# Kernel tuning notes

Measured on AMD Instinct MI355X. Metric: run time of the kernel, lower is better.

Reference implementation:

```python
import jax, jax.numpy as jnp
import numpy as np

B, N, D, K, S = 256, 100000, 768, 5, 256
EPS = 1e-8  # F.cosine_similarity eps


def setup_inputs() -> dict:
    key = jax.random.key(0)
    ks = jax.random.split(key, 6)
    content_features = jax.random.normal(ks[0], (B, D), jnp.float32)
    target_speaker_id = jax.random.randint(ks[1], (B,), 0, S, dtype=jnp.int64)
    training_features = jax.random.normal(ks[2], (N, D), jnp.float32)
    speaker_ids = jax.random.randint(ks[3], (N,), 0, S, dtype=jnp.int64)
    W1 = jax.random.normal(ks[4], (2 * D, D), jnp.float32) * 0.02
    b1 = jnp.zeros((D,), jnp.float32)
    W2 = jax.random.normal(ks[5], (D, D), jnp.float32) * 0.02
    b2 = jnp.zeros((D,), jnp.float32)
    return {
        "content_features": content_features,
        "target_speaker_id": target_speaker_id,
        "training_features": training_features,
        "speaker_ids": speaker_ids,
        "W1": W1, "b1": b1, "W2": W2, "b2": b2,
    }


def reference(content_features, target_speaker_id, training_features, speaker_ids, W1, b1, W2, b2):
    # Cosine similarity of each query against the full memory bank (vectorized
    # version of the per-sample torch loop; speaker mask applied via -inf fill).
    qn = content_features / jnp.maximum(
        jnp.linalg.norm(content_features, axis=-1, keepdims=True), EPS)
    cn = training_features / jnp.maximum(
        jnp.linalg.norm(training_features, axis=-1, keepdims=True), EPS)
    sims = jnp.einsum('bd,nd->bn', qn, cn)                     # [B, N]
    same_spk = speaker_ids[None, :] == target_speaker_id[:, None]  # [B, N]
    masked = jnp.where(same_spk, sims, jnp.float32(-1e30))
    _, top_idx = jax.lax.top_k(masked, K)                      # [B, K]
    retrieved = training_features[top_idx].mean(axis=1)        # [B, D]
    combined = jnp.concatenate([content_features, retrieved], axis=-1)  # [B, 2D]
    # enhance_net (dropout p=0.05 is identity at inference)
    h = jax.nn.silu(combined @ W1 + b1)
    enhanced = h @ W2 + b2
    # Samples with no same-speaker candidate pass through unchanged.
    has_match = same_spk.any(axis=1, keepdims=True)
    return jnp.where(has_match, enhanced, content_features)
```

## Files before the change

kernel.cpp:

```cpp
#include <hip/hip_runtime.h>
#include <hip/hip_bf16.h>
#include <math.h>

#define DIM 768
#define KSEL 5
#define NSPK 256
#define BCAP 2048
#define GSPLIT 8
#define NSLICE (GSPLIT * 4)
#define SK1 16
#define SK2 12
#define SCAT_ITEMS 4

__global__ __launch_bounds__(1024)
void scatter_hist_kernel(const int* __restrict__ spk, int n,
                         int* __restrict__ cursor, int* __restrict__ bucket) {
    __shared__ int hist[NSPK];
    __shared__ int base[NSPK];
    const int tid = threadIdx.x;
    const int i0  = blockIdx.x * (1024 * SCAT_ITEMS);

    if (tid < NSPK) hist[tid] = 0;
    __syncthreads();

    int s_[SCAT_ITEMS], r_[SCAT_ITEMS];
#pragma unroll
    for (int j = 0; j < SCAT_ITEMS; ++j) {
        int i = i0 + tid + j * 1024;
        if (i < n) {
            int s = spk[i];
            s_[j] = s;
            r_[j] = atomicAdd(&hist[s], 1);
        } else {
            s_[j] = -1; r_[j] = 0;
        }
    }
    __syncthreads();

    if (tid < NSPK) base[tid] = hist[tid] ? atomicAdd(&cursor[tid], hist[tid]) : 0;
    __syncthreads();

#pragma unroll
    for (int j = 0; j < SCAT_ITEMS; ++j) {
        int i = i0 + tid + j * 1024;
        if (i < n) {
            int s = s_[j];
            int p = base[s] + r_[j];
            if (p < BCAP) bucket[(size_t)s * BCAP + p] = i;
        }
    }
}

__global__ __launch_bounds__(256)
void topk_partial_kernel(const float* __restrict__ content,
                         const int* __restrict__ target_spk,
                         const float* __restrict__ train,
                         const int* __restrict__ counts,
                         const int* __restrict__ bucket,
                         float* __restrict__ pvals,
                         int* __restrict__ pidx) {
    const int b    = blockIdx.x;
    const int g    = blockIdx.y;
    const int tid  = threadIdx.x;
    const int lane = tid & 63;
    const int wave = tid >> 6;
    const int slice = g * 4 + wave;

    const float4* q4 = (const float4*)(content + (size_t)b * DIM);
    const float4 q0 = q4[lane], q1 = q4[lane + 64], q2 = q4[lane + 128];

    const int spk = target_spk[b];
    const int cnt = min(counts[spk], BCAP);
    const int* buck = bucket + (size_t)spk * BCAP;

    float tv[KSEL] = {-3.0e38f, -3.0e38f, -3.0e38f, -3.0e38f, -3.0e38f};
    int   ti[KSEL] = {-1, -1, -1, -1, -1};

    int c = slice;
    int rowA = (c < cnt) ? buck[c] : -1;
    int rowB = (c + NSLICE < cnt) ? buck[c + NSLICE] : -1;

    for (; c < cnt; c += 2 * NSLICE) {
        const int curA = rowA;
        const int curB = rowB;
        const bool has2 = (curB >= 0);
        const float4* ra = (const float4*)(train + (size_t)curA * DIM);
        const float4* rb = (const float4*)(train + (size_t)(has2 ? curB : curA) * DIM);

        float4 a0 = ra[lane], a1 = ra[lane + 64], a2 = ra[lane + 128];
        float4 b0 = rb[lane], b1 = rb[lane + 64], b2 = rb[lane + 128];

        const int cn = c + 2 * NSLICE;
        rowA = (cn < cnt) ? buck[cn] : -1;
        rowB = (cn + NSLICE < cnt) ? buck[cn + NSLICE] : -1;

        float dA = 0.f, cA = 0.f, dB = 0.f, cB = 0.f;
        dA += a0.x*q0.x + a0.y*q0.y + a0.z*q0.z + a0.w*q0.w;
        cA += a0.x*a0.x + a0.y*a0.y + a0.z*a0.z + a0.w*a0.w;
        dB += b0.x*q0.x + b0.y*q0.y + b0.z*q0.z + b0.w*q0.w;
        cB += b0.x*b0.x + b0.y*b0.y + b0.z*b0.z + b0.w*b0.w;
        dA += a1.x*q1.x + a1.y*q1.y + a1.z*q1.z + a1.w*q1.w;
        cA += a1.x*a1.x + a1.y*a1.y + a1.z*a1.z + a1.w*a1.w;
        dB += b1.x*q1.x + b1.y*q1.y + b1.z*q1.z + b1.w*q1.w;
        cB += b1.x*b1.x + b1.y*b1.y + b1.z*b1.z + b1.w*b1.w;
        dA += a2.x*q2.x + a2.y*q2.y + a2.z*q2.z + a2.w*q2.w;
        cA += a2.x*a2.x + a2.y*a2.y + a2.z*a2.z + a2.w*a2.w;
        dB += b2.x*q2.x + b2.y*q2.y + b2.z*q2.z + b2.w*q2.w;
        cB += b2.x*b2.x + b2.y*b2.y + b2.z*b2.z + b2.w*b2.w;

#pragma unroll
        for (int off = 32; off; off >>= 1) {
            dA += __shfl_xor(dA, off);
            cA += __shfl_xor(cA, off);
            dB += __shfl_xor(dB, off);
            cB += __shfl_xor(cB, off);
        }
        const float keyA = dA * rsqrtf(cA);
        const float keyB = dB * rsqrtf(cB);

        if (keyA > tv[KSEL - 1]) {
#pragma unroll
            for (int j = 0; j < KSEL; ++j)
                if (keyA > tv[j]) {
                    for (int m = KSEL - 1; m > j; --m) { tv[m] = tv[m-1]; ti[m] = ti[m-1]; }
                    tv[j] = keyA; ti[j] = curA;
                    break;
                }
        }
        if (has2 && keyB > tv[KSEL - 1]) {
#pragma unroll
            for (int j = 0; j < KSEL; ++j)
                if (keyB > tv[j]) {
                    for (int m = KSEL - 1; m > j; --m) { tv[m] = tv[m-1]; ti[m] = ti[m-1]; }
                    tv[j] = keyB; ti[j] = curB;
                    break;
                }
        }
    }

    if (lane == 0) {
        float* pv = pvals + ((size_t)b * NSLICE + slice) * KSEL;
        int*   pi = pidx  + ((size_t)b * NSLICE + slice) * KSEL;
#pragma unroll
        for (int j = 0; j < KSEL; ++j) { pv[j] = tv[j]; pi[j] = ti[j]; }
    }
}

__global__ __launch_bounds__(256)
void merge_retrieve_kernel(const float* __restrict__ content,
                           const int* __restrict__ target_spk,
                           const float* __restrict__ train,
                           const int* __restrict__ spk_ids,
                           const int* __restrict__ counts,
                           const float* __restrict__ pvals,
                           const int* __restrict__ pidx,
                           float* __restrict__ combined,
                           int* __restrict__ flags,
                           int nTrain) {
    __shared__ float mv[NSLICE * KSEL];
    __shared__ int   mi[NSLICE * KSEL];
    __shared__ int   sel[KSEL];
    const int b = blockIdx.x, tid = threadIdx.x;
    const int NP = NSLICE * KSEL;

    for (int i = tid; i < NP; i += 256) {
        mv[i] = pvals[(size_t)b * NP + i];
        mi[i] = pidx[(size_t)b * NP + i];
    }
    __syncthreads();

    if (tid < 64) {
        const int l = tid;
        float L0 = mv[l];
        float L1 = mv[l + 64];
        float L2 = (l < 32) ? mv[l + 128] : -3.4e38f;
#pragma unroll
        for (int j = 0; j < KSEL; ++j) {
            float bv = L0; int code = l;
            if (L1 > bv) { bv = L1; code = l + 64; }
            if (L2 > bv) { bv = L2; code = l + 128; }
#pragma unroll
            for (int off = 32; off; off >>= 1) {
                float ov = __shfl_xor(bv, off);
                int   oc = __shfl_xor(code, off);
                if (ov > bv) { bv = ov; code = oc; }
            }
            if ((code & 63) == l) {
                if (code < 64) L0 = -3.4e38f;
                else if (code < 128) L1 = -3.4e38f;
                else L2 = -3.4e38f;
            }
            if (l == 0) sel[j] = (bv > -1.0e37f) ? mi[code] : -1;
        }
    }
    __syncthreads();

    if (tid == 0) {
        const int spk = target_spk[b];
        const int cnt = counts[spk];
        flags[b] = (cnt > 0) ? 1 : 0;
        if (cnt < KSEL) {
            int fill = 0;
            for (int j = 0; j < KSEL; ++j) if (sel[j] < 0) {
                while (fill < nTrain && spk_ids[fill] == spk) ++fill;
                sel[j] = (fill < nTrain) ? fill : 0;
                ++fill;
            }
        }
    }
    __syncthreads();

    const int s0 = sel[0], s1 = sel[1], s2 = sel[2], s3 = sel[3], s4 = sel[4];
    const float* qrow = content + (size_t)b * DIM;
    float* crow = combined + (size_t)b * 2 * DIM;
    for (int d = tid; d < DIM; d += 256) {
        float acc = train[(size_t)s0 * DIM + d] + train[(size_t)s1 * DIM + d]
                  + train[(size_t)s2 * DIM + d] + train[(size_t)s3 * DIM + d]
                  + train[(size_t)s4 * DIM + d];
        crow[d]       = qrow[d];
        crow[DIM + d] = acc * 0.2f;
    }
}

__global__ __launch_bounds__(256)
void gemm_partial_kernel(const float* __restrict__ A, const float* __restrict__ W,
                         float* __restrict__ part, int M, int Nc, int Kd, int KS) {
    __shared__ float As[32][68];
    __shared__ float Ws[32][68];
    const int tid  = threadIdx.x;
    const int col0 = blockIdx.x * 64;
    const int row0 = blockIdx.y * 64;
    const int sk   = blockIdx.z;
    const int kbase = sk * KS;
    const int ty4 = (tid >> 4) << 2;
    const int tx4 = (tid & 15) << 2;

    float acc[4][4] = {};

    for (int kt = 0; kt < KS; kt += 32) {
        const int k0 = kbase + kt;
#pragma unroll
        for (int i = 0; i < 2; ++i) {
            int idx = tid + 256 * i;
            int r   = idx >> 3;
            int kq  = (idx & 7) << 2;
            float4 v = *(const float4*)&A[(size_t)(row0 + r) * Kd + k0 + kq];
            As[kq + 0][r] = v.x; As[kq + 1][r] = v.y;
            As[kq + 2][r] = v.z; As[kq + 3][r] = v.w;
        }
#pragma unroll
        for (int i = 0; i < 2; ++i) {
            int idx = tid + 256 * i;
            int kr  = idx >> 4;
            int c4  = (idx & 15) << 2;
            *(float4*)&Ws[kr][c4] = *(const float4*)&W[(size_t)(k0 + kr) * Nc + col0 + c4];
        }
        __syncthreads();
#pragma unroll
        for (int k = 0; k < 32; ++k) {
            float4 av = *(const float4*)&As[k][ty4];
            float4 wv = *(const float4*)&Ws[k][tx4];
            float a_[4] = {av.x, av.y, av.z, av.w};
            float w_[4] = {wv.x, wv.y, wv.z, wv.w};
#pragma unroll
            for (int i = 0; i < 4; ++i)
#pragma unroll
                for (int j = 0; j < 4; ++j) acc[i][j] += a_[i] * w_[j];
        }
        __syncthreads();
    }

    float* p = part + ((size_t)sk * M + row0) * Nc + col0;
#pragma unroll
    for (int i = 0; i < 4; ++i) {
        float4 o = make_float4(acc[i][0], acc[i][1], acc[i][2], acc[i][3]);
        *(float4*)&p[(size_t)(ty4 + i) * Nc + tx4] = o;
    }
}

template <int ACT, bool SELECT, int NSK>
__global__ __launch_bounds__(256)
void combine_kernel(const float* __restrict__ part, const float* __restrict__ bias,
                    float* __restrict__ out, int M, int Nc,
                    const int* __restrict__ flags, const float* __restrict__ pass) {
    const int i = blockIdx.x * 256 + threadIdx.x;
    if (i >= M * Nc) return;
    const int row = i / Nc;
    const int col = i - row * Nc;
    float v = bias[col];
#pragma unroll
    for (int s = 0; s < NSK; ++s) v += part[(size_t)s * M * Nc + i];
    if (ACT == 1) v = v / (1.0f + expf(-v));
    if (SELECT && !flags[row]) v = pass[i];
    out[i] = v;
}

extern "C" void kernel_launch(void* const* d_in, const int* in_sizes, int n_in,
                              void* d_out, int out_size, void* d_ws, size_t ws_size,
                              hipStream_t stream) {
    const float* content = (const float*)d_in[0];
    const int*   target  = (const int*)d_in[1];
    const float* train   = (const float*)d_in[2];
    const int*   spk     = (const int*)d_in[3];
    const float* W1      = (const float*)d_in[4];
    const float* b1      = (const float*)d_in[5];
    const float* W2      = (const float*)d_in[6];
    const float* b2      = (const float*)d_in[7];
    float* out = (float*)d_out;

    const int B = in_sizes[1];
    const int N = in_sizes[3];

    char* w = (char*)d_ws;
    size_t off = 0;
    auto alloc = [&](size_t bytes) -> void* {
        off = (off + 255) & ~(size_t)255;
        void* p = w + off;
        off += bytes;
        return p;
    };
    int*   cursor   = (int*)alloc(NSPK * sizeof(int));
    int*   bucket   = (int*)alloc((size_t)NSPK * BCAP * sizeof(int));
    int*   flags    = (int*)alloc((size_t)B * sizeof(int));
    float* pvals    = (float*)alloc((size_t)B * NSLICE * KSEL * sizeof(float));
    int*   pidx     = (int*)alloc((size_t)B * NSLICE * KSEL * sizeof(int));
    float* combined = (float*)alloc((size_t)B * 2 * DIM * sizeof(float));
    float* hbuf     = (float*)alloc((size_t)B * DIM * sizeof(float));
    float* part1    = (float*)alloc((size_t)SK1 * B * DIM * sizeof(float));
    float* part2    = (float*)alloc((size_t)SK2 * B * DIM * sizeof(float));
    (void)ws_size;

    hipMemsetAsync(cursor, 0, NSPK * sizeof(int), stream);
    const int scat_blocks = (N + 1024 * SCAT_ITEMS - 1) / (1024 * SCAT_ITEMS);
    scatter_hist_kernel<<<scat_blocks, 1024, 0, stream>>>(spk, N, cursor, bucket);

    topk_partial_kernel<<<dim3(B, GSPLIT), 256, 0, stream>>>(
        content, target, train, cursor, bucket, pvals, pidx);
    merge_retrieve_kernel<<<B, 256, 0, stream>>>(
        content, target, train, spk, cursor, pvals, pidx, combined, flags, N);

    gemm_partial_kernel<<<dim3(DIM / 64, B / 64, SK1), 256, 0, stream>>>(
        combined, W1, part1, B, DIM, 2 * DIM, 2 * DIM / SK1);
    combine_kernel<1, false, SK1><<<(B * DIM + 255) / 256, 256, 0, stream>>>(
        part1, b1, hbuf, B, DIM, nullptr, nullptr);
    gemm_partial_kernel<<<dim3(DIM / 64, B / 64, SK2), 256, 0, stream>>>(
        hbuf, W2, part2, B, DIM, DIM, DIM / SK2);
    combine_kernel<0, true, SK2><<<(B * DIM + 255) / 256, 256, 0, stream>>>(
        part2, b2, out, B, DIM, flags, content);
}
```

Before: 136.1 us.

## Group queries by speaker so each candidate-row scan serves two queries

The scatter kernel now also builds a per-speaker list of query indices. The top-k kernel is relaunched over speakers instead of queries, and each wave scores two queries of the same speaker against every candidate row it loads. The goal is to cut repeated reads of the same speaker's training rows when several queries share a speaker, and to reuse each row norm across both queries. The cost is uneven work: speakers with no queries exit at once, while speakers with three or more queries loop over their rows again, which can lengthen the critical path.

```diff
diff --git a/kernel.cpp b/kernel.cpp
--- a/kernel.cpp
+++ b/kernel.cpp
@@ -6,6 +6,7 @@
 #define KSEL 5
 #define NSPK 256
 #define BCAP 2048
+#define QCAP 256
 #define GSPLIT 8
 #define NSLICE (GSPLIT * 4)
 #define SK1 16
@@ -14,11 +15,19 @@
 
 __global__ __launch_bounds__(1024)
 void scatter_hist_kernel(const int* __restrict__ spk, int n,
-                         int* __restrict__ cursor, int* __restrict__ bucket) {
+                         int* __restrict__ cursor, int* __restrict__ bucket,
+                         const int* __restrict__ target, int B,
+                         int* __restrict__ qcnt, int* __restrict__ qlist) {
     __shared__ int hist[NSPK];
     __shared__ int base[NSPK];
     const int tid = threadIdx.x;
     const int i0  = blockIdx.x * (1024 * SCAT_ITEMS);
+
+    if (blockIdx.x == 0 && tid < B) {
+        int s = target[tid];
+        int p = atomicAdd(&qcnt[s], 1);
+        qlist[(size_t)s * QCAP + p] = tid;
+    }
 
     if (tid < NSPK) hist[tid] = 0;
     __syncthreads();
@@ -52,97 +61,148 @@
 }
 
 __global__ __launch_bounds__(256)
-void topk_partial_kernel(const float* __restrict__ content,
-                         const int* __restrict__ target_spk,
-                         const float* __restrict__ train,
-                         const int* __restrict__ counts,
-                         const int* __restrict__ bucket,
-                         float* __restrict__ pvals,
-                         int* __restrict__ pidx) {
-    const int b    = blockIdx.x;
-    const int g    = blockIdx.y;
+void topk_spk_kernel(const float* __restrict__ content,
+                     const float* __restrict__ train,
+                     const int* __restrict__ counts,
+                     const int* __restrict__ bucket,
+                     const int* __restrict__ qcnt,
+                     const int* __restrict__ qlist,
+                     float* __restrict__ pvals,
+                     int* __restrict__ pidx) {
+    const int s  = blockIdx.x;
+    const int qn = qcnt[s];
+    if (qn == 0) return;
+
     const int tid  = threadIdx.x;
     const int lane = tid & 63;
     const int wave = tid >> 6;
-    const int slice = g * 4 + wave;
-
-    const float4* q4 = (const float4*)(content + (size_t)b * DIM);
-    const float4 q0 = q4[lane], q1 = q4[lane + 64], q2 = q4[lane + 128];
-
-    const int spk = target_spk[b];
-    const int cnt = min(counts[spk], BCAP);
-    const int* buck = bucket + (size_t)spk * BCAP;
-
-    float tv[KSEL] = {-3.0e38f, -3.0e38f, -3.0e38f, -3.0e38f, -3.0e38f};
-    int   ti[KSEL] = {-1, -1, -1, -1, -1};
-
-    int c = slice;
-    int rowA = (c < cnt) ? buck[c] : -1;
-    int rowB = (c + NSLICE < cnt) ? buck[c + NSLICE] : -1;
-
-    for (; c < cnt; c += 2 * NSLICE) {
-        const int curA = rowA;
-        const int curB = rowB;
-        const bool has2 = (curB >= 0);
-        const float4* ra = (const float4*)(train + (size_t)curA * DIM);
-        const float4* rb = (const float4*)(train + (size_t)(has2 ? curB : curA) * DIM);
-
-        float4 a0 = ra[lane], a1 = ra[lane + 64], a2 = ra[lane + 128];
-        float4 b0 = rb[lane], b1 = rb[lane + 64], b2 = rb[lane + 128];
-
-        const int cn = c + 2 * NSLICE;
-        rowA = (cn < cnt) ? buck[cn] : -1;
-        rowB = (cn + NSLICE < cnt) ? buck[cn + NSLICE] : -1;
-
-        float dA = 0.f, cA = 0.f, dB = 0.f, cB = 0.f;
-        dA += a0.x*q0.x + a0.y*q0.y + a0.z*q0.z + a0.w*q0.w;
-        cA += a0.x*a0.x + a0.y*a0.y + a0.z*a0.z + a0.w*a0.w;
-        dB += b0.x*q0.x + b0.y*q0.y + b0.z*q0.z + b0.w*q0.w;
-        cB += b0.x*b0.x + b0.y*b0.y + b0.z*b0.z + b0.w*b0.w;
-        dA += a1.x*q1.x + a1.y*q1.y + a1.z*q1.z + a1.w*q1.w;
-        cA += a1.x*a1.x + a1.y*a1.y + a1.z*a1.z + a1.w*a1.w;
-        dB += b1.x*q1.x + b1.y*q1.y + b1.z*q1.z + b1.w*q1.w;
-        cB += b1.x*b1.x + b1.y*b1.y + b1.z*b1.z + b1.w*b1.w;
-        dA += a2.x*q2.x + a2.y*q2.y + a2.z*q2.z + a2.w*q2.w;
-        cA += a2.x*a2.x + a2.y*a2.y + a2.z*a2.z + a2.w*a2.w;
-        dB += b2.x*q2.x + b2.y*q2.y + b2.z*q2.z + b2.w*q2.w;
-        cB += b2.x*b2.x + b2.y*b2.y + b2.z*b2.z + b2.w*b2.w;
-
-#pragma unroll
-        for (int off = 32; off; off >>= 1) {
-            dA += __shfl_xor(dA, off);
-            cA += __shfl_xor(cA, off);
-            dB += __shfl_xor(dB, off);
-            cB += __shfl_xor(cB, off);
-        }
-        const float keyA = dA * rsqrtf(cA);
-        const float keyB = dB * rsqrtf(cB);
-
-        if (keyA > tv[KSEL - 1]) {
-#pragma unroll
-            for (int j = 0; j < KSEL; ++j)
-                if (keyA > tv[j]) {
-                    for (int m = KSEL - 1; m > j; --m) { tv[m] = tv[m-1]; ti[m] = ti[m-1]; }
-                    tv[j] = keyA; ti[j] = curA;
-                    break;
+    const int slice = blockIdx.y * 4 + wave;
+
+    const int cnt = min(counts[s], BCAP);
+    const int* buck = bucket + (size_t)s * BCAP;
+
+    for (int c0 = 0; c0 < qn; c0 += 2) {
+        const int bq0   = qlist[(size_t)s * QCAP + c0];
+        const bool hasq1 = (c0 + 1 < qn);
+        const int bq1   = hasq1 ? qlist[(size_t)s * QCAP + c0 + 1] : bq0;
+
+        const float4* q0p = (const float4*)(content + (size_t)bq0 * DIM);
+        const float4* q1p = (const float4*)(content + (size_t)bq1 * DIM);
+        const float4 p0 = q0p[lane], p1 = q0p[lane + 64], p2 = q0p[lane + 128];
+        const float4 r0 = q1p[lane], r1 = q1p[lane + 64], r2 = q1p[lane + 128];
+
+        float tv0[KSEL] = {-3.0e38f, -3.0e38f, -3.0e38f, -3.0e38f, -3.0e38f};
+        int   ti0[KSEL] = {-1, -1, -1, -1, -1};
+        float tv1[KSEL] = {-3.0e38f, -3.0e38f, -3.0e38f, -3.0e38f, -3.0e38f};
+        int   ti1[KSEL] = {-1, -1, -1, -1, -1};
+
+        int c = slice;
+        int rowA = (c < cnt) ? buck[c] : -1;
+        int rowB = (c + NSLICE < cnt) ? buck[c + NSLICE] : -1;
+
+        for (; c < cnt; c += 2 * NSLICE) {
+            const int curA = rowA;
+            const int curB = rowB;
+            const bool has2 = (curB >= 0);
+            const float4* ra = (const float4*)(train + (size_t)curA * DIM);
+            const float4* rb = (const float4*)(train + (size_t)(has2 ? curB : curA) * DIM);
+
+            float4 xa0 = ra[lane], xa1 = ra[lane + 64], xa2 = ra[lane + 128];
+            float4 xb0 = rb[lane], xb1 = rb[lane + 64], xb2 = rb[lane + 128];
+
+            const int cn = c + 2 * NSLICE;
+            rowA = (cn < cnt) ? buck[cn] : -1;
+            rowB = (cn + NSLICE < cnt) ? buck[cn + NSLICE] : -1;
+
+            float dA0 = 0.f, dA1 = 0.f, cA = 0.f;
+            float dB0 = 0.f, dB1 = 0.f, cB = 0.f;
+
+            dA0 += xa0.x*p0.x + xa0.y*p0.y + xa0.z*p0.z + xa0.w*p0.w;
+            dA1 += xa0.x*r0.x + xa0.y*r0.y + xa0.z*r0.z + xa0.w*r0.w;
+            cA  += xa0.x*xa0.x + xa0.y*xa0.y + xa0.z*xa0.z + xa0.w*xa0.w;
+            dB0 += xb0.x*p0.x + xb0.y*p0.y + xb0.z*p0.z + xb0.w*p0.w;
+            dB1 += xb0.x*r0.x + xb0.y*r0.y + xb0.z*r0.z + xb0.w*r0.w;
+            cB  += xb0.x*xb0.x + xb0.y*xb0.y + xb0.z*xb0.z + xb0.w*xb0.w;
+
+            dA0 += xa1.x*p1.x + xa1.y*p1.y + xa1.z*p1.z + xa1.w*p1.w;
+            dA1 += xa1.x*r1.x + xa1.y*r1.y + xa1.z*r1.z + xa1.w*r1.w;
+            cA  += xa1.x*xa1.x + xa1.y*xa1.y + xa1.z*xa1.z + xa1.w*xa1.w;
+            dB0 += xb1.x*p1.x + xb1.y*p1.y + xb1.z*p1.z + xb1.w*p1.w;
+            dB1 += xb1.x*r1.x + xb1.y*r1.y + xb1.z*r1.z + xb1.w*r1.w;
+            cB  += xb1.x*xb1.x + xb1.y*xb1.y + xb1.z*xb1.z + xb1.w*xb1.w;
+
+            dA0 += xa2.x*p2.x + xa2.y*p2.y + xa2.z*p2.z + xa2.w*p2.w;
+            dA1 += xa2.x*r2.x + xa2.y*r2.y + xa2.z*r2.z + xa2.w*r2.w;
+            cA  += xa2.x*xa2.x + xa2.y*xa2.y + xa2.z*xa2.z + xa2.w*xa2.w;
+            dB0 += xb2.x*p2.x + xb2.y*p2.y + xb2.z*p2.z + xb2.w*p2.w;
+            dB1 += xb2.x*r2.x + xb2.y*r2.y + xb2.z*r2.z + xb2.w*r2.w;
+            cB  += xb2.x*xb2.x + xb2.y*xb2.y + xb2.z*xb2.z + xb2.w*xb2.w;
+
+#pragma unroll
+            for (int off = 32; off; off >>= 1) {
+                dA0 += __shfl_xor(dA0, off);
+                dA1 += __shfl_xor(dA1, off);
+                cA  += __shfl_xor(cA,  off);
+                dB0 += __shfl_xor(dB0, off);
+                dB1 += __shfl_xor(dB1, off);
+                cB  += __shfl_xor(cB,  off);
+            }
+            const float irA = rsqrtf(cA), irB = rsqrtf(cB);
+            const float keyA0 = dA0 * irA, keyA1 = dA1 * irA;
+            const float keyB0 = dB0 * irB, keyB1 = dB1 * irB;
+
+            if (keyA0 > tv0[KSEL - 1]) {
+#pragma unroll
+                for (int j = 0; j < KSEL; ++j)
+                    if (keyA0 > tv0[j]) {
+                        for (int m = KSEL - 1; m > j; --m) { tv0[m] = tv0[m-1]; ti0[m] = ti0[m-1]; }
+                        tv0[j] = keyA0; ti0[j] = curA;
+                        break;
+                    }
+            }
+            if (has2 && keyB0 > tv0[KSEL - 1]) {
+#pragma unroll
+                for (int j = 0; j < KSEL; ++j)
+                    if (keyB0 > tv0[j]) {
+                        for (int m = KSEL - 1; m > j; --m) { tv0[m] = tv0[m-1]; ti0[m] = ti0[m-1]; }
+                        tv0[j] = keyB0; ti0[j] = curB;
+                        break;
+                    }
+            }
+            if (hasq1) {
+                if (keyA1 > tv1[KSEL - 1]) {
+#pragma unroll
+                    for (int j = 0; j < KSEL; ++j)
+                        if (keyA1 > tv1[j]) {
+                            for (int m = KSEL - 1; m > j; --m) { tv1[m] = tv1[m-1]; ti1[m] = ti1[m-1]; }
+                            tv1[j] = keyA1; ti1[j] = curA;
+                            break;
+                        }
                 }
-        }
-        if (has2 && keyB > tv[KSEL - 1]) {
-#pragma unroll
-            for (int j = 0; j < KSEL; ++j)
-                if (keyB > tv[j]) {
-                    for (int m = KSEL - 1; m > j; --m) { tv[m] = tv[m-1]; ti[m] = ti[m-1]; }
-                    tv[j] = keyB; ti[j] = curB;
-                    break;
+                if (has2 && keyB1 > tv1[KSEL - 1]) {
+#pragma unroll
+                    for (int j = 0; j < KSEL; ++j)
+                        if (keyB1 > tv1[j]) {
+                            for (int m = KSEL - 1; m > j; --m) { tv1[m] = tv1[m-1]; ti1[m] = ti1[m-1]; }
+                            tv1[j] = keyB1; ti1[j] = curB;
+                            break;
+                        }
                 }
-        }
-    }
-
-    if (lane == 0) {
-        float* pv = pvals + ((size_t)b * NSLICE + slice) * KSEL;
-        int*   pi = pidx  + ((size_t)b * NSLICE + slice) * KSEL;
-#pragma unroll
-        for (int j = 0; j < KSEL; ++j) { pv[j] = tv[j]; pi[j] = ti[j]; }
+            }
+        }
+
+        if (lane == 0) {
+            float* pv = pvals + ((size_t)bq0 * NSLICE + slice) * KSEL;
+            int*   pi = pidx  + ((size_t)bq0 * NSLICE + slice) * KSEL;
+#pragma unroll
+            for (int j = 0; j < KSEL; ++j) { pv[j] = tv0[j]; pi[j] = ti0[j]; }
+            if (hasq1) {
+                float* pv1 = pvals + ((size_t)bq1 * NSLICE + slice) * KSEL;
+                int*   pi1 = pidx  + ((size_t)bq1 * NSLICE + slice) * KSEL;
+#pragma unroll
+                for (int j = 0; j < KSEL; ++j) { pv1[j] = tv1[j]; pi1[j] = ti1[j]; }
+            }
+        }
     }
 }
 
@@ -320,6 +380,8 @@
         return p;
     };
     int*   cursor   = (int*)alloc(NSPK * sizeof(int));
+    int*   qcnt     = (int*)alloc(NSPK * sizeof(int));
+    int*   qlist    = (int*)alloc((size_t)NSPK * QCAP * sizeof(int));
     int*   bucket   = (int*)alloc((size_t)NSPK * BCAP * sizeof(int));
     int*   flags    = (int*)alloc((size_t)B * sizeof(int));
     float* pvals    = (float*)alloc((size_t)B * NSLICE * KSEL * sizeof(float));
@@ -330,12 +392,13 @@
     float* part2    = (float*)alloc((size_t)SK2 * B * DIM * sizeof(float));
     (void)ws_size;
 
-    hipMemsetAsync(cursor, 0, NSPK * sizeof(int), stream);
+    hipMemsetAsync(cursor, 0, 2 * NSPK * sizeof(int), stream);
     const int scat_blocks = (N + 1024 * SCAT_ITEMS - 1) / (1024 * SCAT_ITEMS);
-    scatter_hist_kernel<<<scat_blocks, 1024, 0, stream>>>(spk, N, cursor, bucket);
-
-    topk_partial_kernel<<<dim3(B, GSPLIT), 256, 0, stream>>>(
-        content, target, train, cursor, bucket, pvals, pidx);
+    scatter_hist_kernel<<<scat_blocks, 1024, 0, stream>>>(spk, N, cursor, bucket,
+                                                          target, B, qcnt, qlist);
+
+    topk_spk_kernel<<<dim3(NSPK, GSPLIT), 256, 0, stream>>>(
+        content, train, cursor, bucket, qcnt, qlist, pvals, pidx);
     merge_retrieve_kernel<<<B, 256, 0, stream>>>(
         content, target, train, spk, cursor, pvals, pidx, combined, flags, N);
 
```

Result: slower. 167.6 us (+23.1%).

## Enlarge GEMM register tile to 128x96 with register-prefetched k-tiles

Applied to the files above, without the earlier changes.

Rewrites the split-K FP32 GEMM to compute a 128x96 output tile per block, with an 8x6 micro-tile per thread instead of 4x4, and a k-step of 16. The next k-tile's global loads are issued into registers before the current tile is computed, overlapping memory latency with FMAs. The second GEMM's split-K factor changes to 16, so its K slice becomes 48. Higher arithmetic intensity per LDS read comes at the cost of more registers and fewer blocks (8x2x16 = 256 per GEMM), which may lower occupancy.

```diff
diff --git a/kernel.cpp b/kernel.cpp
--- a/kernel.cpp
+++ b/kernel.cpp
@@ -9,7 +9,7 @@
 #define GSPLIT 8
 #define NSLICE (GSPLIT * 4)
 #define SK1 16
-#define SK2 12
+#define SK2 16
 #define SCAT_ITEMS 4
 
 __global__ __launch_bounds__(1024)
@@ -225,56 +225,82 @@
 __global__ __launch_bounds__(256)
 void gemm_partial_kernel(const float* __restrict__ A, const float* __restrict__ W,
                          float* __restrict__ part, int M, int Nc, int Kd, int KS) {
-    __shared__ float As[32][68];
-    __shared__ float Ws[32][68];
+    __shared__ float As[16][132];
+    __shared__ float Ws[16][100];
     const int tid  = threadIdx.x;
-    const int col0 = blockIdx.x * 64;
-    const int row0 = blockIdx.y * 64;
+    const int col0 = blockIdx.x * 96;
+    const int row0 = blockIdx.y * 128;
     const int sk   = blockIdx.z;
     const int kbase = sk * KS;
+    const int nt = KS >> 4;
+
     const int ty4 = (tid >> 4) << 2;
-    const int tx4 = (tid & 15) << 2;
-
-    float acc[4][4] = {};
-
-    for (int kt = 0; kt < KS; kt += 32) {
-        const int k0 = kbase + kt;
-#pragma unroll
-        for (int i = 0; i < 2; ++i) {
-            int idx = tid + 256 * i;
-            int r   = idx >> 3;
-            int kq  = (idx & 7) << 2;
-            float4 v = *(const float4*)&A[(size_t)(row0 + r) * Kd + k0 + kq];
-            As[kq + 0][r] = v.x; As[kq + 1][r] = v.y;
-            As[kq + 2][r] = v.z; As[kq + 3][r] = v.w;
-        }
-#pragma unroll
-        for (int i = 0; i < 2; ++i) {
-            int idx = tid + 256 * i;
-            int kr  = idx >> 4;
-            int c4  = (idx & 15) << 2;
-            *(float4*)&Ws[kr][c4] = *(const float4*)&W[(size_t)(k0 + kr) * Nc + col0 + c4];
-        }
+    const int tx  = tid & 15;
+    const int tx4 = tx << 2;
+    const int tx2 = tx << 1;
+
+    const int ra0 = tid >> 2;
+    const int ka0 = (tid & 3) << 2;
+    const int ra1 = ra0 + 64;
+    const int kw0 = tid / 24;
+    const int cw0 = (tid % 24) << 2;
+    const int tid2 = tid + 256;
+    const int kw1 = tid2 / 24;
+    const int cw1 = (tid2 % 24) << 2;
+    const bool wv = (tid < 128);
+
+    float4 a0, a1, w0, w1;
+    {
+        const int kb = kbase;
+        a0 = *(const float4*)&A[(size_t)(row0 + ra0) * Kd + kb + ka0];
+        a1 = *(const float4*)&A[(size_t)(row0 + ra1) * Kd + kb + ka0];
+        w0 = *(const float4*)&W[(size_t)(kb + kw0) * Nc + col0 + cw0];
+        if (wv) w1 = *(const float4*)&W[(size_t)(kb + kw1) * Nc + col0 + cw1];
+    }
+
+    float acc[8][6] = {};
+
+    for (int t = 0; t < nt; ++t) {
         __syncthreads();
-#pragma unroll
-        for (int k = 0; k < 32; ++k) {
-            float4 av = *(const float4*)&As[k][ty4];
-            float4 wv = *(const float4*)&Ws[k][tx4];
-            float a_[4] = {av.x, av.y, av.z, av.w};
-            float w_[4] = {wv.x, wv.y, wv.z, wv.w};
-#pragma unroll
-            for (int i = 0; i < 4; ++i)
-#pragma unroll
-                for (int j = 0; j < 4; ++j) acc[i][j] += a_[i] * w_[j];
+        As[ka0 + 0][ra0] = a0.x; As[ka0 + 1][ra0] = a0.y;
+        As[ka0 + 2][ra0] = a0.z; As[ka0 + 3][ra0] = a0.w;
+        As[ka0 + 0][ra1] = a1.x; As[ka0 + 1][ra1] = a1.y;
+        As[ka0 + 2][ra1] = a1.z; As[ka0 + 3][ra1] = a1.w;
+        *(float4*)&Ws[kw0][cw0] = w0;
+        if (wv) *(float4*)&Ws[kw1][cw1] = w1;
+
+        if (t + 1 < nt) {
+            const int kb = kbase + (t + 1) * 16;
+            a0 = *(const float4*)&A[(size_t)(row0 + ra0) * Kd + kb + ka0];
+            a1 = *(const float4*)&A[(size_t)(row0 + ra1) * Kd + kb + ka0];
+            w0 = *(const float4*)&W[(size_t)(kb + kw0) * Nc + col0 + cw0];
+            if (wv) w1 = *(const float4*)&W[(size_t)(kb + kw1) * Nc + col0 + cw1];
         }
         __syncthreads();
+
+#pragma unroll
+        for (int k = 0; k < 16; ++k) {
+            float4 av0 = *(const float4*)&As[k][ty4];
+            float4 av1 = *(const float4*)&As[k][ty4 + 64];
+            float4 wv0 = *(const float4*)&Ws[k][tx4];
+            float2 wv1 = *(const float2*)&Ws[k][64 + tx2];
+            const float a_[8] = {av0.x, av0.y, av0.z, av0.w, av1.x, av1.y, av1.z, av1.w};
+            const float w_[6] = {wv0.x, wv0.y, wv0.z, wv0.w, wv1.x, wv1.y};
+#pragma unroll
+            for (int i = 0; i < 8; ++i)
+#pragma unroll
+                for (int j = 0; j < 6; ++j) acc[i][j] += a_[i] * w_[j];
+        }
     }
 
     float* p = part + ((size_t)sk * M + row0) * Nc + col0;
 #pragma unroll
-    for (int i = 0; i < 4; ++i) {
-        float4 o = make_float4(acc[i][0], acc[i][1], acc[i][2], acc[i][3]);
-        *(float4*)&p[(size_t)(ty4 + i) * Nc + tx4] = o;
+    for (int i = 0; i < 8; ++i) {
+        const int row = ty4 + (i & 3) + ((i >> 2) << 6);
+        float4 o4 = make_float4(acc[i][0], acc[i][1], acc[i][2], acc[i][3]);
+        *(float4*)&p[(size_t)row * Nc + tx4] = o4;
+        float2 o2 = make_float2(acc[i][4], acc[i][5]);
+        *(float2*)&p[(size_t)row * Nc + 64 + tx2] = o2;
     }
 }
 
@@ -339,11 +365,11 @@
     merge_retrieve_kernel<<<B, 256, 0, stream>>>(
         content, target, train, spk, cursor, pvals, pidx, combined, flags, N);
 
-    gemm_partial_kernel<<<dim3(DIM / 64, B / 64, SK1), 256, 0, stream>>>(
+    gemm_partial_kernel<<<dim3(DIM / 96, B / 128, SK1), 256, 0, stream>>>(
         combined, W1, part1, B, DIM, 2 * DIM, 2 * DIM / SK1);
     combine_kernel<1, false, SK1><<<(B * DIM + 255) / 256, 256, 0, stream>>>(
         part1, b1, hbuf, B, DIM, nullptr, nullptr);
-    gemm_partial_kernel<<<dim3(DIM / 64, B / 64, SK2), 256, 0, stream>>>(
+    gemm_partial_kernel<<<dim3(DIM / 96, B / 128, SK2), 256, 0, stream>>>(
         hbuf, W2, part2, B, DIM, DIM, DIM / SK2);
     combine_kernel<0, true, SK2><<<(B * DIM + 255) / 256, 256, 0, stream>>>(
         part2, b2, out, B, DIM, flags, content);
```

Measured after the change: 138.1 us. Within noise of the previous version (+1.5%).
